# Kernel optimization log

Hardware: AMD Instinct MI355X
Metric: run time of the kernel (lower is better)

Reference implementation:

```python
import jax, jax.numpy as jnp
import numpy as np

N = 100000      # num_nodes
E = 1_600_000   # edges (avg degree 16)
D_IN = 128
D_H = 128
D_OUT = 128


def setup_inputs() -> dict:
    key = jax.random.key(0)
    ks = jax.random.split(key, 11)
    x = jax.random.normal(ks[0], (N, D_IN), dtype=jnp.float32)
    edge_index = jax.random.randint(ks[1], (2, E), 0, N, dtype=jnp.int32)
    s_in = 1.0 / np.sqrt(D_IN)
    s_h = 1.0 / np.sqrt(D_H)
    return {
        "x": x,
        "edge_index": edge_index,
        "W_neigh1": jax.random.uniform(ks[2], (D_H, D_IN), jnp.float32, -s_in, s_in),
        "b_neigh1": jax.random.uniform(ks[3], (D_H,), jnp.float32, -s_in, s_in),
        "W_self1": jax.random.uniform(ks[4], (D_H, D_IN), jnp.float32, -s_in, s_in),
        "b_self1": jax.random.uniform(ks[5], (D_H,), jnp.float32, -s_in, s_in),
        "W_neigh2": jax.random.uniform(ks[6], (D_OUT, D_H), jnp.float32, -s_h, s_h),
        "b_neigh2": jax.random.uniform(ks[7], (D_OUT,), jnp.float32, -s_h, s_h),
        "W_self2": jax.random.uniform(ks[8], (D_OUT, D_H), jnp.float32, -s_h, s_h),
        "b_self2": jax.random.uniform(ks[9], (D_OUT,), jnp.float32, -s_h, s_h),
    }


def reference(x, edge_index, W_neigh1, b_neigh1, W_self1, b_self1,
              W_neigh2, b_neigh2, W_self2, b_self2):
    src, dst = edge_index[0], edge_index[1]
    n = x.shape[0]
    # row-normalized adjacency: deg over dst (row index), clamped to >= 1
    deg = jax.ops.segment_sum(jnp.ones(src.shape[0], x.dtype), dst, num_segments=n)
    inv_deg = 1.0 / jnp.maximum(deg, 1.0)  # [N]

    def agg(h):  # mean aggregation: (A_rownorm @ h)
        return jax.ops.segment_sum(h[src], dst, num_segments=n) * inv_deg[:, None]

    h1 = agg(x) @ W_neigh1.T + b_neigh1 + x @ W_self1.T + b_self1
    h1 = jax.nn.relu(h1)
    # dropout omitted (eval-mode / deterministic reference)
    h2 = agg(h1) @ W_neigh2.T + b_neigh2 + h1 @ W_self2.T + b_self2
    return h2
```

## Files before the change

kernel.cpp:

```cpp
#include <hip/hip_runtime.h>
#include <hip/hip_bf16.h>


typedef __attribute__((ext_vector_type(8))) short short8;
typedef __attribute__((ext_vector_type(4))) float float4_;

#define NBMAX 512

__device__ __forceinline__ unsigned short f2bf(float f) {
    unsigned int u = __float_as_uint(f);
    unsigned int r = (u + 0x7FFFu + ((u >> 16) & 1u)) >> 16;
    return (unsigned short)r;
}

__global__ __launch_bounds__(256) void bucket_count(const int* __restrict__ dst, int E, int NB,
                                                    int* __restrict__ bucketCnt) {
    __shared__ int h[NBMAX];
    int tid = threadIdx.x;
    for (int b = tid; b < NB; b += 256) h[b] = 0;
    __syncthreads();
    int base = blockIdx.x * 4096;
    for (int i = 0; i < 16; i++) {
        int e = base + i * 256 + tid;
        if (e < E) atomicAdd(&h[dst[e] >> 8], 1);
    }
    __syncthreads();
    for (int b = tid; b < NB; b += 256)
        if (h[b]) atomicAdd(&bucketCnt[b], h[b]);
}

__global__ __launch_bounds__(512) void bucket_scan(const int* __restrict__ bucketCnt, int NB,
                                                   int* __restrict__ bucketOffs,
                                                   int* __restrict__ bucketCur) {
    __shared__ int sd[512];
    int t = threadIdx.x;
    int v = (t < NB) ? bucketCnt[t] : 0;
    sd[t] = v;
    __syncthreads();
    for (int off = 1; off < 512; off <<= 1) {
        int x = sd[t];
        int y = (t >= off) ? sd[t - off] : 0;
        __syncthreads();
        sd[t] = x + y;
        __syncthreads();
    }
    int excl = sd[t] - v;
    if (t <= NB) bucketOffs[t] = excl;
    if (t < NB) bucketCur[t] = excl;
}

__global__ __launch_bounds__(256) void partition_wprep(
    const int* __restrict__ src, const int* __restrict__ dst, int E, int NB, int partBlocks,
    int* __restrict__ bucketCur, unsigned int* __restrict__ bucketBuf,
    const float* __restrict__ Wn1, const float* __restrict__ Ws1,
    const float* __restrict__ bn1, const float* __restrict__ bs1,
    const float* __restrict__ Wn2, const float* __restrict__ Ws2,
    const float* __restrict__ bn2, const float* __restrict__ bs2,
    unsigned short* __restrict__ Bpre, float* __restrict__ biasPre) {
    int tid = threadIdx.x;
    if ((int)blockIdx.x >= partBlocks) {
        int wb = blockIdx.x - partBlocks;
        int l = wb >> 4;
        const float* Wn = l ? Wn2 : Wn1;
        const float* Ws = l ? Ws2 : Ws1;
        int fi = (wb & 15) * 256 + tid;
        int kt = fi >> 9;
        int nt = (fi >> 6) & 7;
        int lane = fi & 63;
        int o = nt * 16 + (lane & 15);
        int k = kt * 32 + (lane >> 4) * 8;
        const float* srcp = (k < 128) ? (Wn + o * 128 + k) : (Ws + o * 128 + (k - 128));
        short8 v;
#pragma unroll
        for (int j = 0; j < 8; j++) v[j] = (short)f2bf(srcp[j]);
        ((short8*)(Bpre + (size_t)l * 32768))[fi] = v;
        if ((wb & 15) == 0 && tid < 128) {
            const float* bn = l ? bn2 : bn1;
            const float* bs = l ? bs2 : bs1;
            biasPre[l * 128 + tid] = bn[tid] + bs[tid];
        }
        return;
    }
    __shared__ int cnt[NBMAX];
    __shared__ int base[NBMAX];
    for (int b = tid; b < NB; b += 256) cnt[b] = 0;
    __syncthreads();
    int eb = blockIdx.x * 4096;
    unsigned int pk[16];
    int bk[16], rk[16];
    for (int i = 0; i < 16; i++) {
        int e = eb + i * 256 + tid;
        if (e < E) {
            int d = dst[e];
            bk[i] = d >> 8;
            pk[i] = (unsigned)src[e] | ((unsigned)(d & 255) << 24);
            rk[i] = atomicAdd(&cnt[bk[i]], 1);
        } else {
            bk[i] = -1;
        }
    }
    __syncthreads();
    for (int b = tid; b < NB; b += 256)
        base[b] = cnt[b] ? atomicAdd(&bucketCur[b], cnt[b]) : 0;
    __syncthreads();
    for (int i = 0; i < 16; i++)
        if (bk[i] >= 0) bucketBuf[base[bk[i]] + rk[i]] = pk[i];
}

__global__ __launch_bounds__(256) void csrbuild_cvt(
    const unsigned int* __restrict__ bucketBuf, const int* __restrict__ bucketOffs,
    int N, int NB, int* __restrict__ deg, int* __restrict__ offs, int* __restrict__ sortedSrc,
    const float* __restrict__ xin, unsigned int* __restrict__ xb, int n2) {
    int tid = threadIdx.x;
    if ((int)blockIdx.x >= NB) {
        int cb = blockIdx.x - NB;
        int base = cb * 2048 + tid;
        if (xb) {
#pragma unroll
            for (int i = 0; i < 8; i++) {
                int t = base + i * 256;
                if (t < n2) {
                    float2 v = ((const float2*)xin)[t];
                    xb[t] = (unsigned)f2bf(v.x) | ((unsigned)f2bf(v.y) << 16);
                }
            }
        }
        return;
    }
    __shared__ int h[256];
    __shared__ int sc[256];
    __shared__ int cur[256];
    int b = blockIdx.x;
    int n0 = b << 8;
    int bo = bucketOffs[b];
    int cnt = bucketOffs[b + 1] - bo;
    h[tid] = 0;
    __syncthreads();
    for (int i = tid; i < cnt; i += 256) atomicAdd(&h[bucketBuf[bo + i] >> 24], 1);
    __syncthreads();
    int v = h[tid];
    sc[tid] = v;
    __syncthreads();
    for (int off = 1; off < 256; off <<= 1) {
        int x = sc[tid];
        int y = (tid >= off) ? sc[tid - off] : 0;
        __syncthreads();
        sc[tid] = x + y;
        __syncthreads();
    }
    int excl = sc[tid] - v;
    cur[tid] = bo + excl;
    int n = n0 + tid;
    if (n < N) {
        deg[n] = v;
        offs[n] = bo + excl;
    }
    __syncthreads();
    for (int i = tid; i < cnt; i += 256) {
        unsigned int pv = bucketBuf[bo + i];
        int pos = atomicAdd(&cur[pv >> 24], 1);
        sortedSrc[pos] = (int)(pv & 0xFFFFFFu);
    }
}

__global__ __launch_bounds__(256) void agg_bf16_kernel(
    const unsigned int* __restrict__ srcFeats,
    const int* __restrict__ deg, const int* __restrict__ offs,
    const int* __restrict__ sortedSrc,
    unsigned int* __restrict__ dst, int Nn) {
    int wave = threadIdx.x >> 6, lane = threadIdx.x & 63;
    int n = blockIdx.x * 4 + wave;
    if (n >= Nn) return;
    int d = deg[n], st = offs[n];
    float a0 = 0.f, a1 = 0.f;
    int j = 0;
    for (; j + 16 <= d; j += 16) {
        unsigned int uu[16];
#pragma unroll
        for (int u = 0; u < 16; u++) {
            int s = __builtin_amdgcn_readfirstlane(sortedSrc[st + j + u]);
            uu[u] = (srcFeats + (size_t)s * 64)[lane];
        }
#pragma unroll
        for (int u = 0; u < 16; u++) {
            a0 += __uint_as_float(uu[u] << 16);
            a1 += __uint_as_float(uu[u] & 0xFFFF0000u);
        }
    }
    for (; j + 8 <= d; j += 8) {
        unsigned int uu[8];
#pragma unroll
        for (int u = 0; u < 8; u++) {
            int s = __builtin_amdgcn_readfirstlane(sortedSrc[st + j + u]);
            uu[u] = (srcFeats + (size_t)s * 64)[lane];
        }
#pragma unroll
        for (int u = 0; u < 8; u++) {
            a0 += __uint_as_float(uu[u] << 16);
            a1 += __uint_as_float(uu[u] & 0xFFFF0000u);
        }
    }
    for (; j < d; j++) {
        int s = __builtin_amdgcn_readfirstlane(sortedSrc[st + j]);
        unsigned int u = (srcFeats + (size_t)s * 64)[lane];
        a0 += __uint_as_float(u << 16);
        a1 += __uint_as_float(u & 0xFFFF0000u);
    }
    float inv = 1.0f / (float)max(d, 1);
    dst[(size_t)n * 64 + lane] = (unsigned)f2bf(a0 * inv) | ((unsigned)f2bf(a1 * inv) << 16);
}

__global__ __launch_bounds__(256) void agg_f32_kernel(
    const float* __restrict__ srcFeats,
    const int* __restrict__ deg, const int* __restrict__ offs,
    const int* __restrict__ sortedSrc,
    unsigned int* __restrict__ dst, int Nn) {
    int wave = threadIdx.x >> 6, lane = threadIdx.x & 63;
    int n = blockIdx.x * 4 + wave;
    if (n >= Nn) return;
    int d = deg[n], st = offs[n];
    float a0 = 0.f, a1 = 0.f;
    int j = 0;
    for (; j + 8 <= d; j += 8) {
        float2 v[8];
#pragma unroll
        for (int u = 0; u < 8; u++) {
            int s = __builtin_amdgcn_readfirstlane(sortedSrc[st + j + u]);
            v[u] = ((const float2*)(srcFeats + (size_t)s * 128))[lane];
        }
#pragma unroll
        for (int u = 0; u < 8; u++) {
            a0 += v[u].x;
            a1 += v[u].y;
        }
    }
    for (; j < d; j++) {
        int s = __builtin_amdgcn_readfirstlane(sortedSrc[st + j]);
        float2 v = ((const float2*)(srcFeats + (size_t)s * 128))[lane];
        a0 += v.x;
        a1 += v.y;
    }
    float inv = 1.0f / (float)max(d, 1);
    dst[(size_t)n * 64 + lane] = (unsigned)f2bf(a0 * inv) | ((unsigned)f2bf(a1 * inv) << 16);
}

__global__ __launch_bounds__(256) void gemm_kernel(
    const unsigned short* __restrict__ Aagg, const void* Aself,
    const unsigned short* __restrict__ Bpre, const float* __restrict__ biasPre,
    void* Out, int relu, int selfF32, int outBf16, int Nrows) {
    __shared__ unsigned short ldsB[8 * 8 * 64 * 8];
    __shared__ float biasS[128];
    int tid = threadIdx.x;

#pragma unroll
    for (int i = 0; i < 16; i++) {
        int fi = tid + 256 * i;
        ((short8*)ldsB)[fi] = ((const short8*)Bpre)[fi];
    }
    if (tid < 128) biasS[tid] = biasPre[tid];
    __syncthreads();

    int wave = tid >> 6, lane = tid & 63;
    int quad = lane >> 4, mr = lane & 15;
    int rowBase = blockIdx.x * 128 + wave * 32;

    float4_ acc[2][8];
    float4_ z = {0.f, 0.f, 0.f, 0.f};
    for (int mt = 0; mt < 2; mt++)
        for (int nt = 0; nt < 8; nt++) acc[mt][nt] = z;

    for (int kt = 0; kt < 8; kt++) {
        int kk = (kt & 3) * 32 + quad * 8;
        short8 a[2];
        for (int mt = 0; mt < 2; mt++) {
            int row = rowBase + mt * 16 + mr;
            if (row >= Nrows) row = Nrows - 1;
            if (kt < 4) {
                a[mt] = *(const short8*)(Aagg + (size_t)row * 128 + kk);
            } else if (selfF32) {
                const float* p = (const float*)Aself + (size_t)row * 128 + kk;
                float4_ f0 = *(const float4_*)p;
                float4_ f1 = *(const float4_*)(p + 4);
                short8 t;
#pragma unroll
                for (int j = 0; j < 4; j++) {
                    t[j] = (short)f2bf(f0[j]);
                    t[4 + j] = (short)f2bf(f1[j]);
                }
                a[mt] = t;
            } else {
                a[mt] = *(const short8*)((const unsigned short*)Aself + (size_t)row * 128 + kk);
            }
        }
        for (int nt = 0; nt < 8; nt++) {
            short8 b = *(const short8*)(ldsB + ((size_t)(kt * 8 + nt) * 64 + lane) * 8);
            acc[0][nt] = __builtin_amdgcn_mfma_f32_16x16x32_bf16(a[0], b, acc[0][nt], 0, 0, 0);
            acc[1][nt] = __builtin_amdgcn_mfma_f32_16x16x32_bf16(a[1], b, acc[1][nt], 0, 0, 0);
        }
    }

    for (int mt = 0; mt < 2; mt++) {
        for (int nt = 0; nt < 8; nt++) {
            int col = nt * 16 + mr;
            float bv = biasS[col];
            for (int r = 0; r < 4; r++) {
                int row = rowBase + mt * 16 + quad * 4 + r;
                if (row < Nrows) {
                    float v = acc[mt][nt][r] + bv;
                    if (relu) v = fmaxf(v, 0.f);
                    if (outBf16)
                        ((unsigned short*)Out)[(size_t)row * 128 + col] = f2bf(v);
                    else
                        ((float*)Out)[(size_t)row * 128 + col] = v;
                }
            }
        }
    }
}

extern "C" void kernel_launch(void* const* d_in, const int* in_sizes, int n_in,
                              void* d_out, int out_size, void* d_ws, size_t ws_size,
                              hipStream_t stream) {
    const float* x = (const float*)d_in[0];
    const int* ei = (const int*)d_in[1];
    const float* Wn1 = (const float*)d_in[2];
    const float* bn1 = (const float*)d_in[3];
    const float* Ws1 = (const float*)d_in[4];
    const float* bs1 = (const float*)d_in[5];
    const float* Wn2 = (const float*)d_in[6];
    const float* bn2 = (const float*)d_in[7];
    const float* Ws2 = (const float*)d_in[8];
    const float* bs2 = (const float*)d_in[9];

    const int N = in_sizes[0] / 128;
    const int E = in_sizes[1] / 2;
    const int* srcI = ei;
    const int* dstI = ei + E;
    const int NB = (N + 255) >> 8;

    char* ws = (char*)d_ws;
    size_t off = 0;
    auto alloc = [&](size_t bytes) -> void* {
        void* p = ws + off;
        off += (bytes + 255) & ~(size_t)255;
        return p;
    };
    int* deg = (int*)alloc((size_t)N * 4);
    int* offs = (int*)alloc((size_t)N * 4);
    int* bucketCnt = (int*)alloc((NBMAX + 1) * 4);
    int* bucketOffs = (int*)alloc((NBMAX + 1) * 4);
    int* bucketCur = (int*)alloc((NBMAX + 1) * 4);
    unsigned short* Bpre = (unsigned short*)alloc(2 * 32768 * 2);
    float* biasPre = (float*)alloc(2 * 128 * 4);
    int* sortedSrc = (int*)alloc((size_t)E * 4);
    unsigned short* Aagg = (unsigned short*)alloc((size_t)N * 128 * 2);
    size_t baseNeed = off;
    size_t bf16Buf = ((size_t)N * 128 * 2 + 255) & ~(size_t)255;
    bool bigWs = (ws_size >= baseNeed + 2 * bf16Buf);
    unsigned int* xb = nullptr;
    unsigned short* h1b = nullptr;
    if (bigWs) {
        xb = (unsigned int*)alloc((size_t)N * 128 * 2);
        h1b = (unsigned short*)alloc((size_t)N * 128 * 2);
    }
    unsigned int* bucketBuf = (unsigned int*)Aagg;

    int ebBlocks = (E + 4095) / 4096;
    int n2 = N * 64;
    int cvtBlocks = bigWs ? (n2 + 2047) / 2048 : 0;
    hipMemsetAsync(bucketCnt, 0, (size_t)NB * 4, stream);
    bucket_count<<<ebBlocks, 256, 0, stream>>>(dstI, E, NB, bucketCnt);
    bucket_scan<<<1, 512, 0, stream>>>(bucketCnt, NB, bucketOffs, bucketCur);
    partition_wprep<<<ebBlocks + 32, 256, 0, stream>>>(
        srcI, dstI, E, NB, ebBlocks, bucketCur, bucketBuf,
        Wn1, Ws1, bn1, bs1, Wn2, Ws2, bn2, bs2, Bpre, biasPre);
    csrbuild_cvt<<<NB + cvtBlocks, 256, 0, stream>>>(bucketBuf, bucketOffs, N, NB, deg, offs,
                                                     sortedSrc, x, xb, n2);

    int aggBlocks = (N + 3) / 4;
    int gemmBlocks = (N + 127) / 128;

    if (bigWs) {
        agg_bf16_kernel<<<aggBlocks, 256, 0, stream>>>(xb, deg, offs, sortedSrc,
                                                       (unsigned int*)Aagg, N);
        gemm_kernel<<<gemmBlocks, 256, 0, stream>>>(Aagg, xb, Bpre, biasPre, h1b, 1, 0, 1, N);
        agg_bf16_kernel<<<aggBlocks, 256, 0, stream>>>((const unsigned int*)h1b, deg, offs,
                                                       sortedSrc, (unsigned int*)Aagg, N);
        gemm_kernel<<<gemmBlocks, 256, 0, stream>>>(Aagg, h1b, Bpre + 32768, biasPre + 128,
                                                    d_out, 0, 0, 0, N);
    } else {
        float* h1 = (float*)d_out;
        agg_f32_kernel<<<aggBlocks, 256, 0, stream>>>(x, deg, offs, sortedSrc,
                                                      (unsigned int*)Aagg, N);
        gemm_kernel<<<gemmBlocks, 256, 0, stream>>>(Aagg, x, Bpre, biasPre, h1, 1, 1, 0, N);
        agg_f32_kernel<<<aggBlocks, 256, 0, stream>>>(h1, deg, offs, sortedSrc,
                                                      (unsigned int*)Aagg, N);
        gemm_kernel<<<gemmBlocks, 256, 0, stream>>>(Aagg, h1, Bpre + 32768, biasPre + 128,
                                                    d_out, 0, 1, 0, N);
    }
}
```

Baseline: 350.7 us.

## Slice bf16 feature tables into eight channel slabs with XCC-affine persistent aggregation

```diff
diff --git a/kernel.cpp b/kernel.cpp
--- a/kernel.cpp
+++ b/kernel.cpp
@@ -4,6 +4,7 @@
 
 typedef __attribute__((ext_vector_type(8))) short short8;
 typedef __attribute__((ext_vector_type(4))) float float4_;
+typedef __attribute__((ext_vector_type(4))) unsigned int uint4_;
 
 #define NBMAX 512
 
@@ -31,9 +32,11 @@
 
 __global__ __launch_bounds__(512) void bucket_scan(const int* __restrict__ bucketCnt, int NB,
                                                    int* __restrict__ bucketOffs,
-                                                   int* __restrict__ bucketCur) {
+                                                   int* __restrict__ bucketCur,
+                                                   int* __restrict__ aggCtr) {
     __shared__ int sd[512];
     int t = threadIdx.x;
+    if (t < 16) aggCtr[t] = 0;
     int v = (t < NB) ? bucketCnt[t] : 0;
     sd[t] = v;
     __syncthreads();
@@ -110,20 +113,31 @@
 __global__ __launch_bounds__(256) void csrbuild_cvt(
     const unsigned int* __restrict__ bucketBuf, const int* __restrict__ bucketOffs,
     int N, int NB, int* __restrict__ deg, int* __restrict__ offs, int* __restrict__ sortedSrc,
-    const float* __restrict__ xin, unsigned int* __restrict__ xb, int n2) {
+    const float* __restrict__ xin, unsigned int* __restrict__ xb, int Np) {
     int tid = threadIdx.x;
     if ((int)blockIdx.x >= NB) {
         int cb = blockIdx.x - NB;
-        int base = cb * 2048 + tid;
-        if (xb) {
-#pragma unroll
-            for (int i = 0; i < 8; i++) {
-                int t = base + i * 256;
-                if (t < n2) {
-                    float2 v = ((const float2*)xin)[t];
-                    xb[t] = (unsigned)f2bf(v.x) | ((unsigned)f2bf(v.y) << 16);
-                }
-            }
+        int p = cb * 256 + tid;
+        if (xb && p < Np) {
+            int n = p >> 3;
+            int s = p & 7;
+            const float* xr = xin + (size_t)n * 128 + s * 16;
+            float4_ f0 = *(const float4_*)(xr);
+            float4_ f1 = *(const float4_*)(xr + 4);
+            float4_ f2 = *(const float4_*)(xr + 8);
+            float4_ f3 = *(const float4_*)(xr + 12);
+            uint4_ qa, qb;
+            qa[0] = (unsigned)f2bf(f0[0]) | ((unsigned)f2bf(f0[1]) << 16);
+            qa[1] = (unsigned)f2bf(f0[2]) | ((unsigned)f2bf(f0[3]) << 16);
+            qa[2] = (unsigned)f2bf(f1[0]) | ((unsigned)f2bf(f1[1]) << 16);
+            qa[3] = (unsigned)f2bf(f1[2]) | ((unsigned)f2bf(f1[3]) << 16);
+            qb[0] = (unsigned)f2bf(f2[0]) | ((unsigned)f2bf(f2[1]) << 16);
+            qb[1] = (unsigned)f2bf(f2[2]) | ((unsigned)f2bf(f2[3]) << 16);
+            qb[2] = (unsigned)f2bf(f3[0]) | ((unsigned)f2bf(f3[1]) << 16);
+            qb[3] = (unsigned)f2bf(f3[2]) | ((unsigned)f2bf(f3[3]) << 16);
+            unsigned int* ob = xb + ((size_t)s * N + n) * 8;
+            *(uint4_*)ob = qa;
+            *(uint4_*)(ob + 4) = qb;
         }
         return;
     }
@@ -163,51 +177,75 @@
     }
 }
 
-__global__ __launch_bounds__(256) void agg_bf16_kernel(
-    const unsigned int* __restrict__ srcFeats,
-    const int* __restrict__ deg, const int* __restrict__ offs,
-    const int* __restrict__ sortedSrc,
-    unsigned int* __restrict__ dst, int Nn) {
-    int wave = threadIdx.x >> 6, lane = threadIdx.x & 63;
-    int n = blockIdx.x * 4 + wave;
-    if (n >= Nn) return;
-    int d = deg[n], st = offs[n];
-    float a0 = 0.f, a1 = 0.f;
-    int j = 0;
-    for (; j + 16 <= d; j += 16) {
-        unsigned int uu[16];
-#pragma unroll
-        for (int u = 0; u < 16; u++) {
-            int s = __builtin_amdgcn_readfirstlane(sortedSrc[st + j + u]);
-            uu[u] = (srcFeats + (size_t)s * 64)[lane];
-        }
-#pragma unroll
-        for (int u = 0; u < 16; u++) {
-            a0 += __uint_as_float(uu[u] << 16);
-            a1 += __uint_as_float(uu[u] & 0xFFFF0000u);
-        }
-    }
-    for (; j + 8 <= d; j += 8) {
-        unsigned int uu[8];
-#pragma unroll
-        for (int u = 0; u < 8; u++) {
-            int s = __builtin_amdgcn_readfirstlane(sortedSrc[st + j + u]);
-            uu[u] = (srcFeats + (size_t)s * 64)[lane];
-        }
-#pragma unroll
-        for (int u = 0; u < 8; u++) {
-            a0 += __uint_as_float(uu[u] << 16);
-            a1 += __uint_as_float(uu[u] & 0xFFFF0000u);
-        }
-    }
-    for (; j < d; j++) {
-        int s = __builtin_amdgcn_readfirstlane(sortedSrc[st + j]);
-        unsigned int u = (srcFeats + (size_t)s * 64)[lane];
-        a0 += __uint_as_float(u << 16);
-        a1 += __uint_as_float(u & 0xFFFF0000u);
-    }
-    float inv = 1.0f / (float)max(d, 1);
-    dst[(size_t)n * 64 + lane] = (unsigned)f2bf(a0 * inv) | ((unsigned)f2bf(a1 * inv) << 16);
+#define AGG_CHN 128
+__global__ __launch_bounds__(256) void agg_sliced(
+    const unsigned int* __restrict__ table, const int* __restrict__ deg,
+    const int* __restrict__ offs, const int* __restrict__ sortedSrc,
+    unsigned int* __restrict__ out, int Nn, int* __restrict__ ctr) {
+    __shared__ int eb[4608];
+    __shared__ int chunkS;
+    int tid = threadIdx.x;
+    int xcc;
+    asm volatile("s_getreg_b32 %0, hwreg(HW_REG_XCC_ID)" : "=s"(xcc));
+    int nChunks = (Nn + AGG_CHN - 1) / AGG_CHN;
+    int g = tid & 7;
+    for (int pass = 0; pass < 8; ++pass) {
+        int s = (xcc + pass) & 7;
+        const unsigned int* tb = table + (size_t)s * Nn * 8;
+        unsigned int* ob = out + (size_t)s * Nn * 8;
+        for (;;) {
+            __syncthreads();
+            if (tid == 0) chunkS = atomicAdd(&ctr[s], 1);
+            __syncthreads();
+            int c = chunkS;
+            if (c >= nChunks) break;
+            int n0 = c * AGG_CHN;
+            int last = min(n0 + AGG_CHN, Nn) - 1;
+            int lo = offs[n0];
+            int cnt = offs[last] + deg[last] - lo;
+            bool fits = (cnt <= 4608);
+            if (fits)
+                for (int i = tid; i < cnt; i += 256) eb[i] = sortedSrc[lo + i];
+            __syncthreads();
+#pragma unroll
+            for (int ph = 0; ph < AGG_CHN / 32; ++ph) {
+                int n = n0 + ph * 32 + (tid >> 3);
+                if (n <= last) {
+                    int d = deg[n];
+                    int st = offs[n] - lo;
+                    float a0 = 0.f, a1 = 0.f;
+                    if (fits) {
+                        int j = 0;
+                        for (; j + 8 <= d; j += 8) {
+                            unsigned int v[8];
+#pragma unroll
+                            for (int u = 0; u < 8; ++u)
+                                v[u] = tb[(size_t)eb[st + j + u] * 8 + g];
+#pragma unroll
+                            for (int u = 0; u < 8; ++u) {
+                                a0 += __uint_as_float(v[u] << 16);
+                                a1 += __uint_as_float(v[u] & 0xFFFF0000u);
+                            }
+                        }
+                        for (; j < d; ++j) {
+                            unsigned int u = tb[(size_t)eb[st + j] * 8 + g];
+                            a0 += __uint_as_float(u << 16);
+                            a1 += __uint_as_float(u & 0xFFFF0000u);
+                        }
+                    } else {
+                        for (int j = 0; j < d; ++j) {
+                            unsigned int u = tb[(size_t)sortedSrc[lo + st + j] * 8 + g];
+                            a0 += __uint_as_float(u << 16);
+                            a1 += __uint_as_float(u & 0xFFFF0000u);
+                        }
+                    }
+                    float inv = 1.0f / (float)max(d, 1);
+                    ob[(size_t)n * 8 + g] =
+                        (unsigned)f2bf(a0 * inv) | ((unsigned)f2bf(a1 * inv) << 16);
+                }
+            }
+        }
+    }
 }
 
 __global__ __launch_bounds__(256) void agg_f32_kernel(
@@ -244,10 +282,14 @@
     dst[(size_t)n * 64 + lane] = (unsigned)f2bf(a0 * inv) | ((unsigned)f2bf(a1 * inv) << 16);
 }
 
+__device__ __forceinline__ short8 loadS8s(const unsigned short* base, int Nn, int row, int kk) {
+    return *(const short8*)(base + ((size_t)(kk >> 4) * Nn + (size_t)row) * 16 + (kk & 15));
+}
+
 __global__ __launch_bounds__(256) void gemm_kernel(
     const unsigned short* __restrict__ Aagg, const void* Aself,
     const unsigned short* __restrict__ Bpre, const float* __restrict__ biasPre,
-    void* Out, int relu, int selfF32, int outBf16, int Nrows) {
+    void* Out, int relu, int selfF32, int outBf16, int sliced, int Nrows) {
     __shared__ unsigned short ldsB[8 * 8 * 64 * 8];
     __shared__ float biasS[128];
     int tid = threadIdx.x;
@@ -276,7 +318,8 @@
             int row = rowBase + mt * 16 + mr;
             if (row >= Nrows) row = Nrows - 1;
             if (kt < 4) {
-                a[mt] = *(const short8*)(Aagg + (size_t)row * 128 + kk);
+                a[mt] = sliced ? loadS8s(Aagg, Nrows, row, kk)
+                               : *(const short8*)(Aagg + (size_t)row * 128 + kk);
             } else if (selfF32) {
                 const float* p = (const float*)Aself + (size_t)row * 128 + kk;
                 float4_ f0 = *(const float4_*)p;
@@ -289,7 +332,7 @@
                 }
                 a[mt] = t;
             } else {
-                a[mt] = *(const short8*)((const unsigned short*)Aself + (size_t)row * 128 + kk);
+                a[mt] = loadS8s((const unsigned short*)Aself, Nrows, row, kk);
             }
         }
         for (int nt = 0; nt < 8; nt++) {
@@ -309,7 +352,7 @@
                     float v = acc[mt][nt][r] + bv;
                     if (relu) v = fmaxf(v, 0.f);
                     if (outBf16)
-                        ((unsigned short*)Out)[(size_t)row * 128 + col] = f2bf(v);
+                        ((unsigned short*)Out)[((size_t)nt * Nrows + row) * 16 + mr] = f2bf(v);
                     else
                         ((float*)Out)[(size_t)row * 128 + col] = v;
                 }
@@ -350,6 +393,7 @@
     int* bucketCnt = (int*)alloc((NBMAX + 1) * 4);
     int* bucketOffs = (int*)alloc((NBMAX + 1) * 4);
     int* bucketCur = (int*)alloc((NBMAX + 1) * 4);
+    int* aggCtr = (int*)alloc(16 * 4);
     unsigned short* Bpre = (unsigned short*)alloc(2 * 32768 * 2);
     float* biasPre = (float*)alloc(2 * 128 * 4);
     int* sortedSrc = (int*)alloc((size_t)E * 4);
@@ -366,36 +410,39 @@
     unsigned int* bucketBuf = (unsigned int*)Aagg;
 
     int ebBlocks = (E + 4095) / 4096;
-    int n2 = N * 64;
-    int cvtBlocks = bigWs ? (n2 + 2047) / 2048 : 0;
+    int Np = N * 8;
+    int cvtBlocks = bigWs ? (Np + 255) / 256 : 0;
     hipMemsetAsync(bucketCnt, 0, (size_t)NB * 4, stream);
     bucket_count<<<ebBlocks, 256, 0, stream>>>(dstI, E, NB, bucketCnt);
-    bucket_scan<<<1, 512, 0, stream>>>(bucketCnt, NB, bucketOffs, bucketCur);
+    bucket_scan<<<1, 512, 0, stream>>>(bucketCnt, NB, bucketOffs, bucketCur, aggCtr);
     partition_wprep<<<ebBlocks + 32, 256, 0, stream>>>(
         srcI, dstI, E, NB, ebBlocks, bucketCur, bucketBuf,
         Wn1, Ws1, bn1, bs1, Wn2, Ws2, bn2, bs2, Bpre, biasPre);
     csrbuild_cvt<<<NB + cvtBlocks, 256, 0, stream>>>(bucketBuf, bucketOffs, N, NB, deg, offs,
-                                                     sortedSrc, x, xb, n2);
-
-    int aggBlocks = (N + 3) / 4;
+                                                     sortedSrc, x, xb, Np);
+
     int gemmBlocks = (N + 127) / 128;
+    int aggGrid = 2048;
 
     if (bigWs) {
-        agg_bf16_kernel<<<aggBlocks, 256, 0, stream>>>(xb, deg, offs, sortedSrc,
-                                                       (unsigned int*)Aagg, N);
-        gemm_kernel<<<gemmBlocks, 256, 0, stream>>>(Aagg, xb, Bpre, biasPre, h1b, 1, 0, 1, N);
-        agg_bf16_kernel<<<aggBlocks, 256, 0, stream>>>((const unsigned int*)h1b, deg, offs,
-                                                       sortedSrc, (unsigned int*)Aagg, N);
+        agg_sliced<<<aggGrid, 256, 0, stream>>>(xb, deg, offs, sortedSrc,
+                                                (unsigned int*)Aagg, N, aggCtr);
+        gemm_kernel<<<gemmBlocks, 256, 0, stream>>>(Aagg, xb, Bpre, biasPre, h1b,
+                                                    1, 0, 1, 1, N);
+        agg_sliced<<<aggGrid, 256, 0, stream>>>((const unsigned int*)h1b, deg, offs, sortedSrc,
+                                                (unsigned int*)Aagg, N, aggCtr + 8);
         gemm_kernel<<<gemmBlocks, 256, 0, stream>>>(Aagg, h1b, Bpre + 32768, biasPre + 128,
-                                                    d_out, 0, 0, 0, N);
+                                                    d_out, 0, 0, 0, 1, N);
     } else {
+        int aggBlocks = (N + 3) / 4;
         float* h1 = (float*)d_out;
         agg_f32_kernel<<<aggBlocks, 256, 0, stream>>>(x, deg, offs, sortedSrc,
                                                       (unsigned int*)Aagg, N);
-        gemm_kernel<<<gemmBlocks, 256, 0, stream>>>(Aagg, x, Bpre, biasPre, h1, 1, 1, 0, N);
+        gemm_kernel<<<gemmBlocks, 256, 0, stream>>>(Aagg, x, Bpre, biasPre, h1,
+                                                    1, 1, 0, 0, N);
         agg_f32_kernel<<<aggBlocks, 256, 0, stream>>>(h1, deg, offs, sortedSrc,
                                                       (unsigned int*)Aagg, N);
         gemm_kernel<<<gemmBlocks, 256, 0, stream>>>(Aagg, h1, Bpre + 32768, biasPre + 128,
-                                                    d_out, 0, 1, 0, N);
-    }
-}
+                                                    d_out, 0, 1, 0, 0, N);
+    }
+}
```

New measurement: 783.1 us. 123% more time.

## Fuse mean aggregation and GEMM into persistent per-layer kernel with atomic tile scheduler

Applied to the files above, without the earlier changes.

```diff
diff --git a/kernel.cpp b/kernel.cpp
--- a/kernel.cpp
+++ b/kernel.cpp
@@ -31,9 +31,11 @@
 
 __global__ __launch_bounds__(512) void bucket_scan(const int* __restrict__ bucketCnt, int NB,
                                                    int* __restrict__ bucketOffs,
-                                                   int* __restrict__ bucketCur) {
+                                                   int* __restrict__ bucketCur,
+                                                   int* __restrict__ tileCtr) {
     __shared__ int sd[512];
     int t = threadIdx.x;
+    if (t < 16) tileCtr[t] = 0;
     int v = (t < NB) ? bucketCnt[t] : 0;
     sd[t] = v;
     __syncthreads();
@@ -163,51 +165,125 @@
     }
 }
 
-__global__ __launch_bounds__(256) void agg_bf16_kernel(
-    const unsigned int* __restrict__ srcFeats,
+__global__ __launch_bounds__(512) void fused_layer(
+    const unsigned int* __restrict__ table,
     const int* __restrict__ deg, const int* __restrict__ offs,
     const int* __restrict__ sortedSrc,
-    unsigned int* __restrict__ dst, int Nn) {
-    int wave = threadIdx.x >> 6, lane = threadIdx.x & 63;
-    int n = blockIdx.x * 4 + wave;
-    if (n >= Nn) return;
-    int d = deg[n], st = offs[n];
-    float a0 = 0.f, a1 = 0.f;
-    int j = 0;
-    for (; j + 16 <= d; j += 16) {
-        unsigned int uu[16];
-#pragma unroll
-        for (int u = 0; u < 16; u++) {
-            int s = __builtin_amdgcn_readfirstlane(sortedSrc[st + j + u]);
-            uu[u] = (srcFeats + (size_t)s * 64)[lane];
-        }
-#pragma unroll
-        for (int u = 0; u < 16; u++) {
-            a0 += __uint_as_float(uu[u] << 16);
-            a1 += __uint_as_float(uu[u] & 0xFFFF0000u);
-        }
-    }
-    for (; j + 8 <= d; j += 8) {
-        unsigned int uu[8];
-#pragma unroll
-        for (int u = 0; u < 8; u++) {
-            int s = __builtin_amdgcn_readfirstlane(sortedSrc[st + j + u]);
-            uu[u] = (srcFeats + (size_t)s * 64)[lane];
-        }
-#pragma unroll
-        for (int u = 0; u < 8; u++) {
-            a0 += __uint_as_float(uu[u] << 16);
-            a1 += __uint_as_float(uu[u] & 0xFFFF0000u);
-        }
-    }
-    for (; j < d; j++) {
-        int s = __builtin_amdgcn_readfirstlane(sortedSrc[st + j]);
-        unsigned int u = (srcFeats + (size_t)s * 64)[lane];
-        a0 += __uint_as_float(u << 16);
-        a1 += __uint_as_float(u & 0xFFFF0000u);
-    }
-    float inv = 1.0f / (float)max(d, 1);
-    dst[(size_t)n * 64 + lane] = (unsigned)f2bf(a0 * inv) | ((unsigned)f2bf(a1 * inv) << 16);
+    const unsigned short* __restrict__ Bpre, const float* __restrict__ biasPre,
+    void* Out, int relu, int outBf16, int Nrows, int* __restrict__ ctr) {
+    __shared__ unsigned short ldsB[32768];
+    __shared__ unsigned int ldsA[32 * 64];
+    __shared__ float biasS[128];
+    __shared__ int tileS;
+    int tid = threadIdx.x;
+
+#pragma unroll
+    for (int i = 0; i < 8; i++) {
+        int fi = tid + 512 * i;
+        ((short8*)ldsB)[fi] = ((const short8*)Bpre)[fi];
+    }
+    if (tid < 128) biasS[tid] = biasPre[tid];
+
+    int wave = tid >> 6, lane = tid & 63;
+    int quad = lane >> 4, mr = lane & 15;
+    int nTiles = (Nrows + 31) >> 5;
+    const unsigned short* selfT = (const unsigned short*)table;
+
+    for (;;) {
+        __syncthreads();
+        if (tid == 0) tileS = atomicAdd(ctr, 1);
+        __syncthreads();
+        int t = tileS;
+        if (t >= nTiles) break;
+        int base = t << 5;
+
+        for (int i = 0; i < 4; i++) {
+            int r = wave * 4 + i;
+            int n = base + r;
+            if (n < Nrows) {
+                int d = deg[n], st = offs[n];
+                float a0 = 0.f, a1 = 0.f;
+                int j = 0;
+                for (; j + 16 <= d; j += 16) {
+                    unsigned int uu[16];
+#pragma unroll
+                    for (int u = 0; u < 16; u++) {
+                        int s = __builtin_amdgcn_readfirstlane(sortedSrc[st + j + u]);
+                        uu[u] = (table + (size_t)s * 64)[lane];
+                    }
+#pragma unroll
+                    for (int u = 0; u < 16; u++) {
+                        a0 += __uint_as_float(uu[u] << 16);
+                        a1 += __uint_as_float(uu[u] & 0xFFFF0000u);
+                    }
+                }
+                for (; j + 8 <= d; j += 8) {
+                    unsigned int uu[8];
+#pragma unroll
+                    for (int u = 0; u < 8; u++) {
+                        int s = __builtin_amdgcn_readfirstlane(sortedSrc[st + j + u]);
+                        uu[u] = (table + (size_t)s * 64)[lane];
+                    }
+#pragma unroll
+                    for (int u = 0; u < 8; u++) {
+                        a0 += __uint_as_float(uu[u] << 16);
+                        a1 += __uint_as_float(uu[u] & 0xFFFF0000u);
+                    }
+                }
+                for (; j < d; j++) {
+                    int s = __builtin_amdgcn_readfirstlane(sortedSrc[st + j]);
+                    unsigned int u = (table + (size_t)s * 64)[lane];
+                    a0 += __uint_as_float(u << 16);
+                    a1 += __uint_as_float(u & 0xFFFF0000u);
+                }
+                float inv = 1.0f / (float)max(d, 1);
+                unsigned int pv = (unsigned)f2bf(a0 * inv) | ((unsigned)f2bf(a1 * inv) << 16);
+                ldsA[(r << 6) + (lane ^ ((r & 7) << 2))] = pv;
+            }
+        }
+        __syncthreads();
+
+        int rBase = (wave & 1) << 4;
+        int nt0 = (wave >> 1) << 1;
+        float4_ z = {0.f, 0.f, 0.f, 0.f};
+        float4_ acc[2];
+        acc[0] = z;
+        acc[1] = z;
+        for (int kt = 0; kt < 8; kt++) {
+            int kk = (kt & 3) * 32 + quad * 8;
+            short8 a;
+            if (kt < 4) {
+                int r = rBase + mr;
+                a = *(const short8*)&ldsA[(r << 6) + ((kk >> 1) ^ ((r & 7) << 2))];
+            } else {
+                int row = base + rBase + mr;
+                if (row >= Nrows) row = Nrows - 1;
+                a = *(const short8*)(selfT + (size_t)row * 128 + kk);
+            }
+#pragma unroll
+            for (int q = 0; q < 2; q++) {
+                short8 b = *(const short8*)(ldsB + ((size_t)(kt * 8 + nt0 + q) * 64 + lane) * 8);
+                acc[q] = __builtin_amdgcn_mfma_f32_16x16x32_bf16(a, b, acc[q], 0, 0, 0);
+            }
+        }
+#pragma unroll
+        for (int q = 0; q < 2; q++) {
+            int col = (nt0 + q) * 16 + mr;
+            float bv = biasS[col];
+#pragma unroll
+            for (int rr = 0; rr < 4; rr++) {
+                int row = base + rBase + quad * 4 + rr;
+                if (row < Nrows) {
+                    float v = acc[q][rr] + bv;
+                    if (relu) v = fmaxf(v, 0.f);
+                    if (outBf16)
+                        ((unsigned short*)Out)[(size_t)row * 128 + col] = f2bf(v);
+                    else
+                        ((float*)Out)[(size_t)row * 128 + col] = v;
+                }
+            }
+        }
+    }
 }
 
 __global__ __launch_bounds__(256) void agg_f32_kernel(
@@ -251,7 +327,6 @@
     __shared__ unsigned short ldsB[8 * 8 * 64 * 8];
     __shared__ float biasS[128];
     int tid = threadIdx.x;
-
 #pragma unroll
     for (int i = 0; i < 16; i++) {
         int fi = tid + 256 * i;
@@ -281,13 +356,13 @@
                 const float* p = (const float*)Aself + (size_t)row * 128 + kk;
                 float4_ f0 = *(const float4_*)p;
                 float4_ f1 = *(const float4_*)(p + 4);
-                short8 t;
+                short8 tt;
 #pragma unroll
                 for (int j = 0; j < 4; j++) {
-                    t[j] = (short)f2bf(f0[j]);
-                    t[4 + j] = (short)f2bf(f1[j]);
-                }
-                a[mt] = t;
+                    tt[j] = (short)f2bf(f0[j]);
+                    tt[4 + j] = (short)f2bf(f1[j]);
+                }
+                a[mt] = tt;
             } else {
                 a[mt] = *(const short8*)((const unsigned short*)Aself + (size_t)row * 128 + kk);
             }
@@ -298,7 +373,6 @@
             acc[1][nt] = __builtin_amdgcn_mfma_f32_16x16x32_bf16(a[1], b, acc[1][nt], 0, 0, 0);
         }
     }
-
     for (int mt = 0; mt < 2; mt++) {
         for (int nt = 0; nt < 8; nt++) {
             int col = nt * 16 + mr;
@@ -350,6 +424,7 @@
     int* bucketCnt = (int*)alloc((NBMAX + 1) * 4);
     int* bucketOffs = (int*)alloc((NBMAX + 1) * 4);
     int* bucketCur = (int*)alloc((NBMAX + 1) * 4);
+    int* tileCtr = (int*)alloc(16 * 4);
     unsigned short* Bpre = (unsigned short*)alloc(2 * 32768 * 2);
     float* biasPre = (float*)alloc(2 * 128 * 4);
     int* sortedSrc = (int*)alloc((size_t)E * 4);
@@ -370,25 +445,22 @@
     int cvtBlocks = bigWs ? (n2 + 2047) / 2048 : 0;
     hipMemsetAsync(bucketCnt, 0, (size_t)NB * 4, stream);
     bucket_count<<<ebBlocks, 256, 0, stream>>>(dstI, E, NB, bucketCnt);
-    bucket_scan<<<1, 512, 0, stream>>>(bucketCnt, NB, bucketOffs, bucketCur);
+    bucket_scan<<<1, 512, 0, stream>>>(bucketCnt, NB, bucketOffs, bucketCur, tileCtr);
     partition_wprep<<<ebBlocks + 32, 256, 0, stream>>>(
         srcI, dstI, E, NB, ebBlocks, bucketCur, bucketBuf,
         Wn1, Ws1, bn1, bs1, Wn2, Ws2, bn2, bs2, Bpre, biasPre);
     csrbuild_cvt<<<NB + cvtBlocks, 256, 0, stream>>>(bucketBuf, bucketOffs, N, NB, deg, offs,
                                                      sortedSrc, x, xb, n2);
 
-    int aggBlocks = (N + 3) / 4;
-    int gemmBlocks = (N + 127) / 128;
-
     if (bigWs) {
-        agg_bf16_kernel<<<aggBlocks, 256, 0, stream>>>(xb, deg, offs, sortedSrc,
-                                                       (unsigned int*)Aagg, N);
-        gemm_kernel<<<gemmBlocks, 256, 0, stream>>>(Aagg, xb, Bpre, biasPre, h1b, 1, 0, 1, N);
-        agg_bf16_kernel<<<aggBlocks, 256, 0, stream>>>((const unsigned int*)h1b, deg, offs,
-                                                       sortedSrc, (unsigned int*)Aagg, N);
-        gemm_kernel<<<gemmBlocks, 256, 0, stream>>>(Aagg, h1b, Bpre + 32768, biasPre + 128,
-                                                    d_out, 0, 0, 0, N);
+        fused_layer<<<512, 512, 0, stream>>>(xb, deg, offs, sortedSrc, Bpre, biasPre,
+                                             h1b, 1, 1, N, tileCtr);
+        fused_layer<<<512, 512, 0, stream>>>((const unsigned int*)h1b, deg, offs, sortedSrc,
+                                             Bpre + 32768, biasPre + 128,
+                                             d_out, 0, 0, N, tileCtr + 8);
     } else {
+        int aggBlocks = (N + 3) / 4;
+        int gemmBlocks = (N + 127) / 128;
         float* h1 = (float*)d_out;
         agg_f32_kernel<<<aggBlocks, 256, 0, stream>>>(x, deg, offs, sortedSrc,
                                                       (unsigned int*)Aagg, N);
```

New measurement: 427.3 us. 21.8% more time.

## Replace global atomic bucket offsets with per-block histogram and column scan

Applied to the files above, without the earlier changes.

```diff
diff --git a/kernel.cpp b/kernel.cpp
--- a/kernel.cpp
+++ b/kernel.cpp
@@ -14,7 +14,7 @@
 }
 
 __global__ __launch_bounds__(256) void bucket_count(const int* __restrict__ dst, int E, int NB,
-                                                    int* __restrict__ bucketCnt) {
+                                                    int* __restrict__ hist) {
     __shared__ int h[NBMAX];
     int tid = threadIdx.x;
     for (int b = tid; b < NB; b += 256) h[b] = 0;
@@ -25,13 +25,41 @@
         if (e < E) atomicAdd(&h[dst[e] >> 8], 1);
     }
     __syncthreads();
-    for (int b = tid; b < NB; b += 256)
-        if (h[b]) atomicAdd(&bucketCnt[b], h[b]);
+    int* out = hist + (size_t)blockIdx.x * NB;
+    for (int b = tid; b < NB; b += 256) out[b] = h[b];
+}
+
+__global__ __launch_bounds__(256) void blk_scan(const int* __restrict__ hist, int nblk, int NB,
+                                                int* __restrict__ baseT,
+                                                int* __restrict__ bucketCnt) {
+    __shared__ int sd[256];
+    __shared__ int carryS;
+    int b = blockIdx.x, tid = threadIdx.x;
+    if (tid == 0) carryS = 0;
+    __syncthreads();
+    for (int c0 = 0; c0 < nblk; c0 += 256) {
+        int i = c0 + tid;
+        int v = (i < nblk) ? hist[(size_t)i * NB + b] : 0;
+        sd[tid] = v;
+        __syncthreads();
+        for (int off = 1; off < 256; off <<= 1) {
+            int x = sd[tid];
+            int y = (tid >= off) ? sd[tid - off] : 0;
+            __syncthreads();
+            sd[tid] = x + y;
+            __syncthreads();
+        }
+        int carry = carryS;
+        if (i < nblk) baseT[(size_t)i * NB + b] = carry + sd[tid] - v;
+        __syncthreads();
+        if (tid == 255) carryS = carry + sd[255];
+        __syncthreads();
+    }
+    if (tid == 0) bucketCnt[b] = carryS;
 }
 
 __global__ __launch_bounds__(512) void bucket_scan(const int* __restrict__ bucketCnt, int NB,
-                                                   int* __restrict__ bucketOffs,
-                                                   int* __restrict__ bucketCur) {
+                                                   int* __restrict__ bucketOffs) {
     __shared__ int sd[512];
     int t = threadIdx.x;
     int v = (t < NB) ? bucketCnt[t] : 0;
@@ -46,12 +74,12 @@
     }
     int excl = sd[t] - v;
     if (t <= NB) bucketOffs[t] = excl;
-    if (t < NB) bucketCur[t] = excl;
 }
 
 __global__ __launch_bounds__(256) void partition_wprep(
     const int* __restrict__ src, const int* __restrict__ dst, int E, int NB, int partBlocks,
-    int* __restrict__ bucketCur, unsigned int* __restrict__ bucketBuf,
+    const int* __restrict__ bucketOffs, const int* __restrict__ baseT,
+    unsigned int* __restrict__ bucketBuf,
     const float* __restrict__ Wn1, const float* __restrict__ Ws1,
     const float* __restrict__ bn1, const float* __restrict__ bs1,
     const float* __restrict__ Wn2, const float* __restrict__ Ws2,
@@ -82,8 +110,11 @@
         return;
     }
     __shared__ int cnt[NBMAX];
-    __shared__ int base[NBMAX];
-    for (int b = tid; b < NB; b += 256) cnt[b] = 0;
+    __shared__ int gb[NBMAX];
+    for (int b = tid; b < NB; b += 256) {
+        cnt[b] = 0;
+        gb[b] = bucketOffs[b] + baseT[(size_t)blockIdx.x * NB + b];
+    }
     __syncthreads();
     int eb = blockIdx.x * 4096;
     unsigned int pk[16];
@@ -100,11 +131,8 @@
         }
     }
     __syncthreads();
-    for (int b = tid; b < NB; b += 256)
-        base[b] = cnt[b] ? atomicAdd(&bucketCur[b], cnt[b]) : 0;
-    __syncthreads();
     for (int i = 0; i < 16; i++)
-        if (bk[i] >= 0) bucketBuf[base[bk[i]] + rk[i]] = pk[i];
+        if (bk[i] >= 0) bucketBuf[gb[bk[i]] + rk[i]] = pk[i];
 }
 
 __global__ __launch_bounds__(256) void csrbuild_cvt(
@@ -337,6 +365,7 @@
     const int* srcI = ei;
     const int* dstI = ei + E;
     const int NB = (N + 255) >> 8;
+    const int ebBlocks = (E + 4095) / 4096;
 
     char* ws = (char*)d_ws;
     size_t off = 0;
@@ -349,7 +378,8 @@
     int* offs = (int*)alloc((size_t)N * 4);
     int* bucketCnt = (int*)alloc((NBMAX + 1) * 4);
     int* bucketOffs = (int*)alloc((NBMAX + 1) * 4);
-    int* bucketCur = (int*)alloc((NBMAX + 1) * 4);
+    int* hist = (int*)alloc((size_t)ebBlocks * NB * 4);
+    int* baseT = (int*)alloc((size_t)ebBlocks * NB * 4);
     unsigned short* Bpre = (unsigned short*)alloc(2 * 32768 * 2);
     float* biasPre = (float*)alloc(2 * 128 * 4);
     int* sortedSrc = (int*)alloc((size_t)E * 4);
@@ -365,14 +395,13 @@
     }
     unsigned int* bucketBuf = (unsigned int*)Aagg;
 
-    int ebBlocks = (E + 4095) / 4096;
     int n2 = N * 64;
     int cvtBlocks = bigWs ? (n2 + 2047) / 2048 : 0;
-    hipMemsetAsync(bucketCnt, 0, (size_t)NB * 4, stream);
-    bucket_count<<<ebBlocks, 256, 0, stream>>>(dstI, E, NB, bucketCnt);
-    bucket_scan<<<1, 512, 0, stream>>>(bucketCnt, NB, bucketOffs, bucketCur);
+    bucket_count<<<ebBlocks, 256, 0, stream>>>(dstI, E, NB, hist);
+    blk_scan<<<NB, 256, 0, stream>>>(hist, ebBlocks, NB, baseT, bucketCnt);
+    bucket_scan<<<1, 512, 0, stream>>>(bucketCnt, NB, bucketOffs);
     partition_wprep<<<ebBlocks + 32, 256, 0, stream>>>(
-        srcI, dstI, E, NB, ebBlocks, bucketCur, bucketBuf,
+        srcI, dstI, E, NB, ebBlocks, bucketOffs, baseT, bucketBuf,
         Wn1, Ws1, bn1, bs1, Wn2, Ws2, bn2, bs2, Bpre, biasPre);
     csrbuild_cvt<<<NB + cvtBlocks, 256, 0, stream>>>(bucketBuf, bucketOffs, N, NB, deg, offs,
                                                      sortedSrc, x, xb, n2);
```

Measured after the change: 347.1 us (median of 2 runs). No clear change (-1.0%).
